# Optimization experiments

Measured on AMD Instinct MI355X. Metric: run time of the kernel, lower is better.

The kernel has to match this reference:

```python
import jax, jax.numpy as jnp
import numpy as np

N_HEAD = 16
EPS = 1e-5

def _layernorm(x, g, b):
    m = jnp.mean(x, axis=-1, keepdims=True)
    v = jnp.mean((x - m) ** 2, axis=-1, keepdims=True)
    return (x - m) * jax.lax.rsqrt(v + EPS) * g + b

def _gru_gate(h, X, w, u, bz):
    # w, u: [3, C, C] stacked (r, z, h) matrices; matches torch.tensordot(X, W, dims=1)
    r = jax.nn.sigmoid(X @ w[0] + h @ u[0])
    z = jax.nn.sigmoid(X @ w[1] + h @ u[1] - bz)
    h_next = jnp.tanh(X @ w[2] + (h * r) @ u[2])
    return (1.0 - z) * h + z * h_next

def setup_inputs() -> dict:
    key = jax.random.key(0)
    B, T, C = 4, 1024, 1024
    ks = jax.random.split(key, 32)
    s = 0.02
    inp = {
        'q': jax.random.normal(ks[0], (B, T, C), jnp.float32),
        'k': jax.random.normal(ks[1], (B, T, C), jnp.float32),
        'v': jax.random.normal(ks[2], (B, T, C), jnp.float32),
        'ln1_g': jnp.ones((C,), jnp.float32), 'ln1_b': jnp.zeros((C,), jnp.float32),
        'ln2_g': jnp.ones((C,), jnp.float32), 'ln2_b': jnp.zeros((C,), jnp.float32),
        'Wq': jax.random.normal(ks[3], (C, C), jnp.float32) * s, 'bq': jnp.zeros((C,), jnp.float32),
        'Wk': jax.random.normal(ks[4], (C, C), jnp.float32) * s, 'bk': jnp.zeros((C,), jnp.float32),
        'Wv': jax.random.normal(ks[5], (C, C), jnp.float32) * s, 'bv': jnp.zeros((C,), jnp.float32),
        'Wp': jax.random.normal(ks[6], (C, C), jnp.float32) * s, 'bp': jnp.zeros((C,), jnp.float32),
        'W1': jax.random.normal(ks[7], (C, 2 * C), jnp.float32) * s, 'b1': jnp.zeros((2 * C,), jnp.float32),
        'W2': jax.random.normal(ks[8], (2 * C, C), jnp.float32) * s, 'b2': jnp.zeros((C,), jnp.float32),
        'g1_w': jax.random.normal(ks[9], (3, C, C), jnp.float32) * s,
        'g1_u': jax.random.normal(ks[10], (3, C, C), jnp.float32) * s,
        'g1_bz': jnp.full((C,), 2.0, jnp.float32),  # init_gru_gate_bias
        'g2_w': jax.random.normal(ks[11], (3, C, C), jnp.float32) * s,
        'g2_u': jax.random.normal(ks[12], (3, C, C), jnp.float32) * s,
        'g2_bz': jnp.full((C,), 2.0, jnp.float32),
    }
    return inp

def reference(q, k, v, ln1_g, ln1_b, ln2_g, ln2_b, Wq, bq, Wk, bk, Wv, bv, Wp, bp,
              W1, b1, W2, b2, g1_w, g1_u, g1_bz, g2_w, g2_u, g2_bz):
    B, T, C = q.shape
    D = C // N_HEAD
    qn = _layernorm(q, ln1_g, ln1_b)
    kn = _layernorm(k, ln1_g, ln1_b)
    vn = _layernorm(v, ln1_g, ln1_b)
    qh = (qn @ Wq + bq).reshape(B, T, N_HEAD, D)
    kh = (kn @ Wk + bk).reshape(B, T, N_HEAD, D)
    vh = (vn @ Wv + bv).reshape(B, T, N_HEAD, D)
    att = jnp.einsum('bqhd,bkhd->bhqk', qh, kh) * (1.0 / np.sqrt(D))
    causal = jnp.tril(jnp.ones((T, T), bool))  # mask[-Tq:, :Tk]
    att_scores = jnp.where(causal, att, -jnp.inf)
    att_probs = jax.nn.softmax(att_scores, axis=-1)
    y = jnp.einsum('bhqk,bkhd->bqhd', att_probs, vh).reshape(B, T, C)
    att_out = y @ Wp + bp
    x = _gru_gate(q, att_out, g1_w, g1_u, g1_bz)
    h = _layernorm(x, ln2_g, ln2_b)
    mlp = jax.nn.gelu(h @ W1 + b1, approximate=False) @ W2 + b2
    x = _gru_gate(x, mlp, g2_w, g2_u, g2_bz)
    return (x, att_scores)
```

## Files before the change

### kernel.cpp

```cpp
#include <hip/hip_runtime.h>
#include <math.h>

#define TDIM 1024
#define CDIM 1024
#define NHEAD 16
#define HD 64
#define MROWS 4096

#define MASK_NEG -1.0e30f

typedef __attribute__((ext_vector_type(8))) __bf16 bf16x8;
typedef __attribute__((ext_vector_type(4))) float f32x4;

__device__ __forceinline__ float sigf(float x) { return 1.0f / (1.0f + expf(-x)); }
__device__ __forceinline__ float geluf(float x) { return x * 0.5f * (1.0f + erff(x * 0.7071067811865475f)); }
__device__ __forceinline__ float bf2f(unsigned short u) {
    union { unsigned u; float f; } x; x.u = ((unsigned)u) << 16; return x.f;
}
__device__ __forceinline__ unsigned short f2bf(float f) {
    union { float f; unsigned u; } x; x.f = f;
    unsigned r = x.u + 0x7FFFu + ((x.u >> 16) & 1u);
    return (unsigned short)(r >> 16);
}

__global__ __launch_bounds__(256) void wconv_t(const float* __restrict__ i0,
                                               const float* __restrict__ i1,
                                               const float* __restrict__ i2,
                                               const float* __restrict__ i3,
                                               int gper,
                                               unsigned short* __restrict__ out,
                                               int K, int N) {
    int z = blockIdx.z;
    int sel = z / gper, sub = z % gper;
    const float* ps = sel == 0 ? i0 : sel == 1 ? i1 : sel == 2 ? i2 : i3;
    const float* inb = ps + (size_t)sub * K * N;
    unsigned short* outb = out + (size_t)z * K * N;
    __shared__ float tile[32][33];
    int t = threadIdx.x;
    int r = t >> 3, c = (t & 7) * 4;
    int kb = blockIdx.y * 32, nb = blockIdx.x * 32;
    float4 vv = *(const float4*)(inb + (size_t)(kb + r) * N + nb + c);
    tile[r][c + 0] = vv.x; tile[r][c + 1] = vv.y; tile[r][c + 2] = vv.z; tile[r][c + 3] = vv.w;
    __syncthreads();
    ushort4 o;
    o.x = f2bf(tile[c + 0][r]); o.y = f2bf(tile[c + 1][r]);
    o.z = f2bf(tile[c + 2][r]); o.w = f2bf(tile[c + 3][r]);
    *(ushort4*)(outb + (size_t)(nb + r) * K + kb + c) = o;
}

__global__ __launch_bounds__(256) void f2bf_kernel(const float* __restrict__ in,
                                                   unsigned short* __restrict__ out) {
    size_t i = ((size_t)blockIdx.x * 256 + threadIdx.x) * 4;
    float4 v = *(const float4*)(in + i);
    ushort4 o; o.x = f2bf(v.x); o.y = f2bf(v.y); o.z = f2bf(v.z); o.w = f2bf(v.w);
    *(ushort4*)(out + i) = o;
}

__global__ __launch_bounds__(256) void ln3_kernel(const float* __restrict__ p0,
                                                  const float* __restrict__ p1,
                                                  const float* __restrict__ p2,
                                                  const float* __restrict__ g,
                                                  const float* __restrict__ b,
                                                  unsigned short* __restrict__ out) {
    int row = blockIdx.x, z = blockIdx.y;
    const float* xr = (z == 0 ? p0 : z == 1 ? p1 : p2) + (size_t)row * CDIM;
    int t = threadIdx.x;
    float4 v = *(const float4*)(xr + t * 4);
    __shared__ float red[256];
    red[t] = v.x + v.y + v.z + v.w;
    __syncthreads();
    for (int o = 128; o > 0; o >>= 1) { if (t < o) red[t] += red[t + o]; __syncthreads(); }
    float mean = red[0] * (1.0f / CDIM);
    __syncthreads();
    float dx = v.x - mean, dy = v.y - mean, dz = v.z - mean, dw = v.w - mean;
    red[t] = dx * dx + dy * dy + dz * dz + dw * dw;
    __syncthreads();
    for (int o = 128; o > 0; o >>= 1) { if (t < o) red[t] += red[t + o]; __syncthreads(); }
    float var = red[0] * (1.0f / CDIM);
    float inv = 1.0f / sqrtf(var + 1e-5f);
    float4 gv = *(const float4*)(g + t * 4);
    float4 bv = *(const float4*)(b + t * 4);
    ushort4 o4;
    o4.x = f2bf(dx * inv * gv.x + bv.x);
    o4.y = f2bf(dy * inv * gv.y + bv.y);
    o4.z = f2bf(dz * inv * gv.z + bv.z);
    o4.w = f2bf(dw * inv * gv.w + bv.w);
    *(ushort4*)(out + ((size_t)z * MROWS + row) * CDIM + t * 4) = o4;
}

template <int GELU>
__global__ __launch_bounds__(256) void mfma_gemm(const unsigned short* __restrict__ A0, size_t aStride,
                                                 const unsigned short* __restrict__ Bt0, size_t bStride,
                                                 const float* __restrict__ b0,
                                                 const float* __restrict__ b1,
                                                 const float* __restrict__ b2,
                                                 unsigned short* __restrict__ C0, size_t cStride,
                                                 int M, int N, int K, int outmode) {
    __shared__ unsigned short As[2][128 * 32];
    __shared__ unsigned short Bs[2][128 * 32];
    int z = blockIdx.z;
    const unsigned short* A = A0 + (size_t)z * aStride;
    const unsigned short* Bt = Bt0 + (size_t)z * bStride;
    unsigned short* C = C0 + (size_t)z * cStride;
    const float* bias = z == 0 ? b0 : z == 1 ? b1 : b2;
    int om = (outmode == 3) ? (z == 2 ? 2 : 1) : outmode;

    int t = threadIdx.x;
    int wave = t >> 6, lane = t & 63;
    int nwg = gridDim.x * gridDim.y;
    int hID = blockIdx.y * gridDim.x + blockIdx.x;
    int nl = (hID & 7) * (nwg >> 3) + (hID >> 3);
    int bx = nl % gridDim.x, by = nl / gridDim.x;
    int m0 = by * 128, n0 = bx * 128;
    int wx = wave & 1, wy = wave >> 1;
    int srow = lane >> 2;
    int scol = (lane & 3) * 8;
    int fr = lane & 15;
    int fq = (lane >> 4) * 8;

    f32x4 acc[4][4] = {};

#define STAGE_AB(buf, k0v)                                                                         \
    {                                                                                              \
        _Pragma("unroll")                                                                          \
        for (int i = 0; i < 2; i++) {                                                              \
            int rt = (wave * 2 + i) * 16 + srow;                                                   \
            __builtin_amdgcn_global_load_lds(                                                      \
                (const __attribute__((address_space(1))) void*)(A + (size_t)(m0 + rt) * K + (k0v) + scol), \
                (__attribute__((address_space(3))) void*)(As[buf] + rt * 32 + scol), 16, 0, 0);    \
            __builtin_amdgcn_global_load_lds(                                                      \
                (const __attribute__((address_space(1))) void*)(Bt + (size_t)(n0 + rt) * K + (k0v) + scol), \
                (__attribute__((address_space(3))) void*)(Bs[buf] + rt * 32 + scol), 16, 0, 0);    \
        }                                                                                          \
    }

    STAGE_AB(0, 0);
    int cur = 0;
    for (int k0 = 0; k0 < K; k0 += 32) {
        __syncthreads();
        if (k0 + 32 < K) STAGE_AB(cur ^ 1, k0 + 32);

        bf16x8 af[4], bfr[4];
#pragma unroll
        for (int mi = 0; mi < 4; mi++)
            af[mi] = *(const bf16x8*)(As[cur] + (wy * 64 + mi * 16 + fr) * 32 + fq);
#pragma unroll
        for (int ni = 0; ni < 4; ni++)
            bfr[ni] = *(const bf16x8*)(Bs[cur] + (wx * 64 + ni * 16 + fr) * 32 + fq);
#pragma unroll
        for (int mi = 0; mi < 4; mi++)
#pragma unroll
            for (int ni = 0; ni < 4; ni++)
                acc[mi][ni] = __builtin_amdgcn_mfma_f32_16x16x32_bf16(af[mi], bfr[ni], acc[mi][ni], 0, 0, 0);
        cur ^= 1;
    }
#undef STAGE_AB

    int col_l = lane & 15, quad = lane >> 4;
#pragma unroll
    for (int ni = 0; ni < 4; ni++) {
        int c = n0 + wx * 64 + ni * 16 + col_l;
        float bb = bias ? bias[c] : 0.0f;
#pragma unroll
        for (int mi = 0; mi < 4; mi++) {
#pragma unroll
            for (int r = 0; r < 4; r++) {
                int row = m0 + wy * 64 + mi * 16 + quad * 4 + r;
                float vv = acc[mi][ni][r] + bb;
                if (GELU) vv = geluf(vv);
                size_t idx;
                if (om == 1) {
                    int bI = row >> 10, tt2 = row & 1023, hh = c >> 6, d = c & 63;
                    idx = (((size_t)(bI * NHEAD + hh)) * TDIM + tt2) * HD + d;
                } else if (om == 2) {
                    int bI = row >> 10, tt2 = row & 1023, hh = c >> 6, d = c & 63;
                    idx = (((size_t)(bI * NHEAD + hh)) * HD + d) * TDIM + tt2;
                } else {
                    idx = (size_t)row * N + c;
                }
                C[idx] = f2bf(vv);
            }
        }
    }
}

__global__ __launch_bounds__(256, 4) void attn_fused(const unsigned short* __restrict__ Q,
                                                     const unsigned short* __restrict__ K,
                                                     const unsigned short* __restrict__ Vt,
                                                     float* __restrict__ S,
                                                     unsigned short* __restrict__ Y) {
    int hID = blockIdx.y * gridDim.x + blockIdx.x;
    int nlw = (hID & 7) * 128 + (hID >> 3);
    int qt = nlw & 15, bh = nlw >> 4;
    int q0 = qt * 64;
    int t = threadIdx.x, w = t >> 6, lane = t & 63;
    int l15 = lane & 15, quad = lane >> 4;
    int l7 = lane & 7, l3 = lane >> 3;

    __shared__ unsigned short Ks[2][4096];
    __shared__ unsigned short Vs[2][4096];
    __shared__ unsigned short PsU[4096];

    const unsigned short* Qb = Q + ((size_t)bh * TDIM + q0) * HD;
    const unsigned short* Kb0 = K + (size_t)bh * TDIM * HD;
    const unsigned short* Vtb = Vt + (size_t)bh * HD * TDIM;
    float* Sb = S + (size_t)bh * TDIM * TDIM;

    int dstoff = w * 512 + lane * 8;

    bf16x8 aq[2];
    {
        int qrow = w * 16 + l15;
#pragma unroll
        for (int kk = 0; kk < 2; kk++)
            aq[kk] = *(const bf16x8*)(Qb + (size_t)qrow * HD + kk * 32 + quad * 8);
    }

    float m_run[4], l_run[4];
    f32x4 yacc[4];
#pragma unroll
    for (int r = 0; r < 4; r++) { m_run[r] = MASK_NEG; l_run[r] = 0.f; }
#pragma unroll
    for (int nd = 0; nd < 4; nd++) yacc[nd] = (f32x4){0.f, 0.f, 0.f, 0.f};

    unsigned short* Psw = PsU + w * 1024;

#define STAGE_KV(buf, ktile)                                                                        \
    {                                                                                               \
        _Pragma("unroll")                                                                           \
        for (int it = 0; it < 2; it++) {                                                            \
            int row = it * 32 + w * 8 + l3;                                        \
            __builtin_amdgcn_global_load_lds(                                                       \
                (const __attribute__((address_space(1))) void*)(Kb0 + (size_t)((ktile) * 64 + row) * HD + ((l7 ^ l3) << 3)), \
                (__attribute__((address_space(3))) void*)(Ks[buf] + it * 2048 + dstoff), 16, 0, 0); \
            __builtin_amdgcn_global_load_lds(                                                       \
                (const __attribute__((address_space(1))) void*)(Vtb + (size_t)row * TDIM + (ktile) * 64 + ((l7 ^ l3) << 3)), \
                (__attribute__((address_space(3))) void*)(Vs[buf] + it * 2048 + dstoff), 16, 0, 0); \
        }                                                                                           \
    }

    STAGE_KV(0, 0);
    int cur = 0;

    for (int kt = 0; kt <= qt; kt++) {
        __syncthreads();
        if (kt < qt) STAGE_KV(cur ^ 1, kt + 1);

        f32x4 sA[4];
#pragma unroll
        for (int n = 0; n < 4; n++) sA[n] = (f32x4){0.f, 0.f, 0.f, 0.f};
        __builtin_amdgcn_s_setprio(1);
#pragma unroll
        for (int kk = 0; kk < 2; kk++) {
#pragma unroll
            for (int n = 0; n < 4; n++) {
                int krow = n * 16 + l15;
                bf16x8 bk = *(const bf16x8*)(Ks[cur] + krow * 64 + ((((kk * 64 + quad * 16)) ^ ((krow & 7) << 4)) >> 1));
                sA[n] = __builtin_amdgcn_mfma_f32_16x16x32_bf16(aq[kk], bk, sA[n], 0, 0, 0);
            }
        }
        __builtin_amdgcn_s_setprio(0);

        int kbase = kt * 64;
        bool diag = (kt == qt);
#pragma unroll
        for (int n = 0; n < 4; n++) {
            int kg = kbase + n * 16 + l15;
#pragma unroll
            for (int r = 0; r < 4; r++) {
                int qg = q0 + w * 16 + quad * 4 + r;
                float x = sA[n][r] * 0.125f;
                if (diag && kg > qg) x = MASK_NEG;
                sA[n][r] = x;
                Sb[(size_t)qg * TDIM + kg] = x;
            }
        }

#pragma unroll
        for (int r = 0; r < 4; r++) {
            float m = fmaxf(fmaxf(sA[0][r], sA[1][r]), fmaxf(sA[2][r], sA[3][r]));
            m = fmaxf(m, __shfl_xor(m, 1));
            m = fmaxf(m, __shfl_xor(m, 2));
            m = fmaxf(m, __shfl_xor(m, 4));
            m = fmaxf(m, __shfl_xor(m, 8));
            float mn = fmaxf(m_run[r], m);
            float sc = expf(m_run[r] - mn);
            m_run[r] = mn;
            float ls = 0.f;
#pragma unroll
            for (int n = 0; n < 4; n++) {
                float p = expf(sA[n][r] - mn);
                sA[n][r] = p;
                ls += p;
            }
            ls += __shfl_xor(ls, 1);
            ls += __shfl_xor(ls, 2);
            ls += __shfl_xor(ls, 4);
            ls += __shfl_xor(ls, 8);
            l_run[r] = l_run[r] * sc + ls;
#pragma unroll
            for (int nd = 0; nd < 4; nd++) yacc[nd][r] *= sc;
        }

#pragma unroll
        for (int n = 0; n < 4; n++) {
            int kk2 = n * 16 + l15;
#pragma unroll
            for (int r = 0; r < 4; r++) {
                int qq = quad * 4 + r;
                Psw[qq * 64 + (((kk2 * 2) ^ ((qq & 7) << 4)) >> 1)] = f2bf(sA[n][r]);
            }
        }

        __builtin_amdgcn_s_setprio(1);
#pragma unroll
        for (int kk = 0; kk < 2; kk++) {
            bf16x8 pa = *(const bf16x8*)(Psw + l15 * 64 + ((((kk * 64 + quad * 16)) ^ ((l15 & 7) << 4)) >> 1));
#pragma unroll
            for (int nd = 0; nd < 4; nd++) {
                int dr = nd * 16 + l15;
                bf16x8 bv = *(const bf16x8*)(Vs[cur] + dr * 64 + ((((kk * 64 + quad * 16)) ^ ((dr & 7) << 4)) >> 1));
                yacc[nd] = __builtin_amdgcn_mfma_f32_16x16x32_bf16(pa, bv, yacc[nd], 0, 0, 0);
            }
        }
        __builtin_amdgcn_s_setprio(0);
        cur ^= 1;
    }
#undef STAGE_KV

    int bI = bh >> 4, h = bh & 15;
#pragma unroll
    for (int r = 0; r < 4; r++) {
        float inv = 1.0f / l_run[r];
        int row = bI * TDIM + q0 + w * 16 + quad * 4 + r;
#pragma unroll
        for (int nd = 0; nd < 4; nd++)
            Y[(size_t)row * CDIM + h * HD + nd * 16 + l15] = f2bf(yacc[nd][r] * inv);
    }

    int kfill = (qt + 1) * 64;
    if (kfill < TDIM) {
        float4 m4 = make_float4(MASK_NEG, MASK_NEG, MASK_NEG, MASK_NEG);
        int rr = t >> 4, cc = (t & 15) * 4;
#pragma unroll
        for (int rp = 0; rp < 4; rp++) {
            float* Srow = Sb + (size_t)(q0 + rp * 16 + rr) * TDIM;
            for (int k4 = kfill + cc; k4 < TDIM; k4 += 64)
                *(float4*)(Srow + k4) = m4;
        }
    }
}

__global__ __launch_bounds__(256) void ew_r(const unsigned short* __restrict__ A, int ldA,
                                            const unsigned short* __restrict__ B, int ldB,
                                            const unsigned short* __restrict__ h,
                                            unsigned short* __restrict__ out) {
    int row = blockIdx.x, c = threadIdx.x * 4;
    ushort4 a = *(const ushort4*)(A + (size_t)row * ldA + c);
    ushort4 b = *(const ushort4*)(B + (size_t)row * ldB + c);
    size_t i = (size_t)row * CDIM + c;
    ushort4 hh = *(const ushort4*)(h + i);
    ushort4 o;
    o.x = f2bf(bf2f(hh.x) * sigf(bf2f(a.x) + bf2f(b.x)));
    o.y = f2bf(bf2f(hh.y) * sigf(bf2f(a.y) + bf2f(b.y)));
    o.z = f2bf(bf2f(hh.z) * sigf(bf2f(a.z) + bf2f(b.z)));
    o.w = f2bf(bf2f(hh.w) * sigf(bf2f(a.w) + bf2f(b.w)));
    *(ushort4*)(out + i) = o;
}

template <int F32OUT, int DOLN>
__global__ __launch_bounds__(256) void ew_final2(const unsigned short* __restrict__ A, int ldA,
                                                 const unsigned short* __restrict__ B, int ldB,
                                                 const unsigned short* __restrict__ B3v,
                                                 const unsigned short* __restrict__ h,
                                                 const float* __restrict__ bz,
                                                 void* __restrict__ out,
                                                 const float* __restrict__ lng,
                                                 const float* __restrict__ lnb,
                                                 unsigned short* __restrict__ lnout) {
    int row = blockIdx.x, t = threadIdx.x, c = t * 4;
    size_t ia = (size_t)row * ldA, ib = (size_t)row * ldB;
    size_t i = (size_t)row * CDIM + c;
    ushort4 a2 = *(const ushort4*)(A + ia + 1024 + c);
    ushort4 b2 = *(const ushort4*)(B + ib + 1024 + c);
    ushort4 a3 = *(const ushort4*)(A + ia + 2048 + c);
    ushort4 b3 = *(const ushort4*)(B3v + i);
    ushort4 hh = *(const ushort4*)(h + i);
    float4 bzv = *(const float4*)(bz + c);
    float zz, o0, o1, o2, o3;
    zz = sigf(bf2f(a2.x) + bf2f(b2.x) - bzv.x); o0 = (1.f - zz) * bf2f(hh.x) + zz * tanhf(bf2f(a3.x) + bf2f(b3.x));
    zz = sigf(bf2f(a2.y) + bf2f(b2.y) - bzv.y); o1 = (1.f - zz) * bf2f(hh.y) + zz * tanhf(bf2f(a3.y) + bf2f(b3.y));
    zz = sigf(bf2f(a2.z) + bf2f(b2.z) - bzv.z); o2 = (1.f - zz) * bf2f(hh.z) + zz * tanhf(bf2f(a3.z) + bf2f(b3.z));
    zz = sigf(bf2f(a2.w) + bf2f(b2.w) - bzv.w); o3 = (1.f - zz) * bf2f(hh.w) + zz * tanhf(bf2f(a3.w) + bf2f(b3.w));
    if (F32OUT) {
        *(float4*)((float*)out + i) = make_float4(o0, o1, o2, o3);
    } else {
        ushort4 o; o.x = f2bf(o0); o.y = f2bf(o1); o.z = f2bf(o2); o.w = f2bf(o3);
        *(ushort4*)((unsigned short*)out + i) = o;
    }
    if (DOLN) {
        __shared__ float red[256];
        red[t] = o0 + o1 + o2 + o3;
        __syncthreads();
        for (int o = 128; o > 0; o >>= 1) { if (t < o) red[t] += red[t + o]; __syncthreads(); }
        float mean = red[0] * (1.0f / CDIM);
        __syncthreads();
        float dx = o0 - mean, dy = o1 - mean, dz = o2 - mean, dw = o3 - mean;
        red[t] = dx * dx + dy * dy + dz * dz + dw * dw;
        __syncthreads();
        for (int o = 128; o > 0; o >>= 1) { if (t < o) red[t] += red[t + o]; __syncthreads(); }
        float var = red[0] * (1.0f / CDIM);
        float inv = 1.0f / sqrtf(var + 1e-5f);
        float4 gv = *(const float4*)(lng + c);
        float4 bv = *(const float4*)(lnb + c);
        ushort4 o4;
        o4.x = f2bf(dx * inv * gv.x + bv.x);
        o4.y = f2bf(dy * inv * gv.y + bv.y);
        o4.z = f2bf(dz * inv * gv.z + bv.z);
        o4.w = f2bf(dw * inv * gv.w + bv.w);
        *(ushort4*)(lnout + i) = o4;
    }
}

extern "C" void kernel_launch(void* const* d_in, const int* in_sizes, int n_in,
                              void* d_out, int out_size, void* d_ws, size_t ws_size,
                              hipStream_t stream) {
    const float* q    = (const float*)d_in[0];
    const float* k    = (const float*)d_in[1];
    const float* v    = (const float*)d_in[2];
    const float* ln1g = (const float*)d_in[3];
    const float* ln1b = (const float*)d_in[4];
    const float* ln2g = (const float*)d_in[5];
    const float* ln2b = (const float*)d_in[6];
    const float* Wq   = (const float*)d_in[7];
    const float* bq   = (const float*)d_in[8];
    const float* Wk   = (const float*)d_in[9];
    const float* bk   = (const float*)d_in[10];
    const float* Wv   = (const float*)d_in[11];
    const float* bv   = (const float*)d_in[12];
    const float* Wp   = (const float*)d_in[13];
    const float* bp   = (const float*)d_in[14];
    const float* W1   = (const float*)d_in[15];
    const float* b1   = (const float*)d_in[16];
    const float* W2   = (const float*)d_in[17];
    const float* b2   = (const float*)d_in[18];
    const float* g1w  = (const float*)d_in[19];
    const float* g1u  = (const float*)d_in[20];
    const float* g1bz = (const float*)d_in[21];
    const float* g2w  = (const float*)d_in[22];
    const float* g2u  = (const float*)d_in[23];
    const float* g2bz = (const float*)d_in[24];

    float* out_x = (float*)d_out;
    float* out_s = out_x + (size_t)MROWS * CDIM;

    unsigned short* w = (unsigned short*)d_ws;
    const size_t MM = (size_t)CDIM * CDIM;
    unsigned short* wWq  = w;
    unsigned short* wWp  = w + 3 * MM;
    unsigned short* wW1  = w + 4 * MM;
    unsigned short* wW2  = w + 6 * MM;
    unsigned short* wg1w = w + 8 * MM;
    unsigned short* wg1u = w + 11 * MM;
    unsigned short* wg2w = w + 14 * MM;
    unsigned short* wg2u = w + 17 * MM;
    unsigned short* act = w + 20 * MM;
    const size_t SLOT = (size_t)MROWS * CDIM;
    unsigned short* s0 = act + 0 * SLOT;
    unsigned short* s1 = act + 1 * SLOT;
    unsigned short* s2 = act + 2 * SLOT;
    unsigned short* s3 = act + 3 * SLOT;
    unsigned short* s4 = act + 4 * SLOT;
    unsigned short* s5 = act + 5 * SLOT;
    unsigned short* s6 = act + 6 * SLOT;
    unsigned short* s7 = act + 7 * SLOT;
    unsigned short* s8 = act + 8 * SLOT;
    (void)s4;

    dim3 blk(256);
    dim3 g_gemm(8, 32, 1);
    dim3 g_gemm3(8, 32, 3);
    dim3 g_gemm_w1(16, 32, 1);
    dim3 g_gemm_g(24, 32, 1);
    dim3 g_attn(16, 64);
    dim3 g_ew(MROWS);

    wconv_t<<<dim3(32, 32, 4), blk, 0, stream>>>(Wq, Wk, Wv, Wp, 1, wWq, 1024, 1024);
    wconv_t<<<dim3(32, 32, 12), blk, 0, stream>>>(g1w, g1u, g2w, g2u, 3, wg1w, 1024, 1024);
    wconv_t<<<dim3(64, 32, 1), blk, 0, stream>>>(W1, W1, W1, W1, 1, wW1, 1024, 2048);
    wconv_t<<<dim3(32, 64, 1), blk, 0, stream>>>(W2, W2, W2, W2, 1, wW2, 2048, 1024);
    f2bf_kernel<<<g_ew, blk, 0, stream>>>(q, s6);

    ln3_kernel<<<dim3(MROWS, 3), blk, 0, stream>>>(q, k, v, ln1g, ln1b, s0);
    mfma_gemm<0><<<g_gemm3, blk, 0, stream>>>(s0, SLOT, wWq, MM, bq, bk, bv, s3, SLOT,
                                              MROWS, CDIM, CDIM, 3);

    attn_fused<<<g_attn, blk, 0, stream>>>(s3, s4, s5, out_s, s0);

    mfma_gemm<0><<<g_gemm, blk, 0, stream>>>(s0, 0, wWp, 0, bp, bp, bp, s1, 0,
                                             MROWS, CDIM, CDIM, 0);

    mfma_gemm<0><<<g_gemm_g, blk, 0, stream>>>(s1, 0, wg1w, 0, nullptr, nullptr, nullptr,
                                               s2, 0, MROWS, 3 * CDIM, CDIM, 0);
    mfma_gemm<0><<<g_gemm_w1, blk, 0, stream>>>(s6, 0, wg1u, 0, nullptr, nullptr, nullptr,
                                                s0, 0, MROWS, 2 * CDIM, CDIM, 0);
    ew_r<<<g_ew, blk, 0, stream>>>(s2, 3 * CDIM, s0, 2 * CDIM, s6, s5);
    mfma_gemm<0><<<g_gemm, blk, 0, stream>>>(s5, 0, wg1u + 2 * MM, 0, nullptr, nullptr, nullptr,
                                             s7, 0, MROWS, CDIM, CDIM, 0);
    ew_final2<0, 1><<<g_ew, blk, 0, stream>>>(s2, 3 * CDIM, s0, 2 * CDIM, s7, s6, g1bz,
                                              s5, ln2g, ln2b, s8);

    mfma_gemm<1><<<g_gemm_w1, blk, 0, stream>>>(s8, 0, wW1, 0, b1, b1, b1, s0, 0,
                                                MROWS, 2 * CDIM, CDIM, 0);
    mfma_gemm<0><<<g_gemm, blk, 0, stream>>>(s0, 0, wW2, 0, b2, b2, b2, s6, 0,
                                             MROWS, CDIM, 2 * CDIM, 0);

    mfma_gemm<0><<<g_gemm_g, blk, 0, stream>>>(s6, 0, wg2w, 0, nullptr, nullptr, nullptr,
                                               s0, 0, MROWS, 3 * CDIM, CDIM, 0);
    mfma_gemm<0><<<g_gemm_w1, blk, 0, stream>>>(s5, 0, wg2u, 0, nullptr, nullptr, nullptr,
                                                s3, 0, MROWS, 2 * CDIM, CDIM, 0);
    ew_r<<<g_ew, blk, 0, stream>>>(s0, 3 * CDIM, s3, 2 * CDIM, s5, s7);
    mfma_gemm<0><<<g_gemm, blk, 0, stream>>>(s7, 0, wg2u + 2 * MM, 0, nullptr, nullptr, nullptr,
                                             s8, 0, MROWS, CDIM, CDIM, 0);
    ew_final2<1, 0><<<g_ew, blk, 0, stream>>>(s0, 3 * CDIM, s3, 2 * CDIM, s8, s5, g2bz,
                                              out_x, nullptr, nullptr, nullptr);
}
```

Baseline: 909.8 us.

## Batch independent GEMMs via per-z descriptor kernel and fuse q bf16 conversion into LN

Replaces the templated GEMM with a descriptor-driven kernel in which each grid z-slice has its own A, B, bias, output, stride, layout mode and GELU flag. Independent GEMMs are merged into single launches: the QKV projections together with the h@U_r/U_z products of gate 1, and the W1 MLP GEMM together with the gate-2 h@U_r/U_z products. The q-to-bf16 conversion is folded into the layernorm kernel, and the buffers are reassigned so the gate products are written to separate contiguous slots. The aim is fewer launches and larger grids that fill the GPU better, at the cost of runtime branching on GELU and layout mode in the GEMM epilogue.

Result: no change. 909.5 us (-0.0%).

```diff
diff --git a/kernel.cpp b/kernel.cpp
--- a/kernel.cpp
+++ b/kernel.cpp
@@ -48,24 +48,21 @@
     *(ushort4*)(outb + (size_t)(nb + r) * K + kb + c) = o;
 }
 
-__global__ __launch_bounds__(256) void f2bf_kernel(const float* __restrict__ in,
-                                                   unsigned short* __restrict__ out) {
-    size_t i = ((size_t)blockIdx.x * 256 + threadIdx.x) * 4;
-    float4 v = *(const float4*)(in + i);
-    ushort4 o; o.x = f2bf(v.x); o.y = f2bf(v.y); o.z = f2bf(v.z); o.w = f2bf(v.w);
-    *(ushort4*)(out + i) = o;
-}
-
 __global__ __launch_bounds__(256) void ln3_kernel(const float* __restrict__ p0,
                                                   const float* __restrict__ p1,
                                                   const float* __restrict__ p2,
                                                   const float* __restrict__ g,
                                                   const float* __restrict__ b,
-                                                  unsigned short* __restrict__ out) {
+                                                  unsigned short* __restrict__ out,
+                                                  unsigned short* __restrict__ qb) {
     int row = blockIdx.x, z = blockIdx.y;
     const float* xr = (z == 0 ? p0 : z == 1 ? p1 : p2) + (size_t)row * CDIM;
     int t = threadIdx.x;
     float4 v = *(const float4*)(xr + t * 4);
+    if (z == 0) {
+        ushort4 o; o.x = f2bf(v.x); o.y = f2bf(v.y); o.z = f2bf(v.z); o.w = f2bf(v.w);
+        *(ushort4*)(qb + (size_t)row * CDIM + t * 4) = o;
+    }
     __shared__ float red[256];
     red[t] = v.x + v.y + v.z + v.w;
     __syncthreads();
@@ -88,22 +85,31 @@
     *(ushort4*)(out + ((size_t)z * MROWS + row) * CDIM + t * 4) = o4;
 }
 
-template <int GELU>
-__global__ __launch_bounds__(256) void mfma_gemm(const unsigned short* __restrict__ A0, size_t aStride,
-                                                 const unsigned short* __restrict__ Bt0, size_t bStride,
-                                                 const float* __restrict__ b0,
-                                                 const float* __restrict__ b1,
-                                                 const float* __restrict__ b2,
-                                                 unsigned short* __restrict__ C0, size_t cStride,
-                                                 int M, int N, int K, int outmode) {
+struct GemmZ {
+    const unsigned short* A;
+    const unsigned short* Bt;
+    const float* bias;
+    unsigned short* C;
+    int ldC;
+    int om;
+    int gelu;
+    int pad;
+};
+struct GemmDesc { GemmZ z0, z1, z2, z3, z4; };
+
+__global__ __launch_bounds__(256) void mfma_gemmz(GemmDesc d, int M, int N, int K) {
     __shared__ unsigned short As[2][128 * 32];
     __shared__ unsigned short Bs[2][128 * 32];
-    int z = blockIdx.z;
-    const unsigned short* A = A0 + (size_t)z * aStride;
-    const unsigned short* Bt = Bt0 + (size_t)z * bStride;
-    unsigned short* C = C0 + (size_t)z * cStride;
-    const float* bias = z == 0 ? b0 : z == 1 ? b1 : b2;
-    int om = (outmode == 3) ? (z == 2 ? 2 : 1) : outmode;
+    GemmZ zz;
+    switch (blockIdx.z) {
+        case 0: zz = d.z0; break;
+        case 1: zz = d.z1; break;
+        case 2: zz = d.z2; break;
+        case 3: zz = d.z3; break;
+        default: zz = d.z4; break;
+    }
+    const unsigned short* A = zz.A;
+    const unsigned short* Bt = zz.Bt;
 
     int t = threadIdx.x;
     int wave = t >> 6, lane = t & 63;
@@ -160,25 +166,25 @@
 #pragma unroll
     for (int ni = 0; ni < 4; ni++) {
         int c = n0 + wx * 64 + ni * 16 + col_l;
-        float bb = bias ? bias[c] : 0.0f;
+        float bb = zz.bias ? zz.bias[c] : 0.0f;
 #pragma unroll
         for (int mi = 0; mi < 4; mi++) {
 #pragma unroll
             for (int r = 0; r < 4; r++) {
                 int row = m0 + wy * 64 + mi * 16 + quad * 4 + r;
                 float vv = acc[mi][ni][r] + bb;
-                if (GELU) vv = geluf(vv);
+                if (zz.gelu) vv = geluf(vv);
                 size_t idx;
-                if (om == 1) {
-                    int bI = row >> 10, tt2 = row & 1023, hh = c >> 6, d = c & 63;
-                    idx = (((size_t)(bI * NHEAD + hh)) * TDIM + tt2) * HD + d;
-                } else if (om == 2) {
-                    int bI = row >> 10, tt2 = row & 1023, hh = c >> 6, d = c & 63;
-                    idx = (((size_t)(bI * NHEAD + hh)) * HD + d) * TDIM + tt2;
+                if (zz.om == 1) {
+                    int bI = row >> 10, tt2 = row & 1023, hh = c >> 6, dd = c & 63;
+                    idx = (((size_t)(bI * NHEAD + hh)) * TDIM + tt2) * HD + dd;
+                } else if (zz.om == 2) {
+                    int bI = row >> 10, tt2 = row & 1023, hh = c >> 6, dd = c & 63;
+                    idx = (((size_t)(bI * NHEAD + hh)) * HD + dd) * TDIM + tt2;
                 } else {
-                    idx = (size_t)row * N + c;
+                    idx = (size_t)row * zz.ldC + c;
                 }
-                C[idx] = f2bf(vv);
+                zz.C[idx] = f2bf(vv);
             }
         }
     }
@@ -351,14 +357,14 @@
     }
 }
 
-__global__ __launch_bounds__(256) void ew_r(const unsigned short* __restrict__ A, int ldA,
-                                            const unsigned short* __restrict__ B, int ldB,
+__global__ __launch_bounds__(256) void ew_r(const unsigned short* __restrict__ A1, int ldA,
+                                            const unsigned short* __restrict__ B1,
                                             const unsigned short* __restrict__ h,
                                             unsigned short* __restrict__ out) {
     int row = blockIdx.x, c = threadIdx.x * 4;
-    ushort4 a = *(const ushort4*)(A + (size_t)row * ldA + c);
-    ushort4 b = *(const ushort4*)(B + (size_t)row * ldB + c);
+    ushort4 a = *(const ushort4*)(A1 + (size_t)row * ldA + c);
     size_t i = (size_t)row * CDIM + c;
+    ushort4 b = *(const ushort4*)(B1 + i);
     ushort4 hh = *(const ushort4*)(h + i);
     ushort4 o;
     o.x = f2bf(bf2f(hh.x) * sigf(bf2f(a.x) + bf2f(b.x)));
@@ -370,7 +376,7 @@
 
 template <int F32OUT, int DOLN>
 __global__ __launch_bounds__(256) void ew_final2(const unsigned short* __restrict__ A, int ldA,
-                                                 const unsigned short* __restrict__ B, int ldB,
+                                                 const unsigned short* __restrict__ B2p,
                                                  const unsigned short* __restrict__ B3v,
                                                  const unsigned short* __restrict__ h,
                                                  const float* __restrict__ bz,
@@ -379,10 +385,10 @@
                                                  const float* __restrict__ lnb,
                                                  unsigned short* __restrict__ lnout) {
     int row = blockIdx.x, t = threadIdx.x, c = t * 4;
-    size_t ia = (size_t)row * ldA, ib = (size_t)row * ldB;
+    size_t ia = (size_t)row * ldA;
     size_t i = (size_t)row * CDIM + c;
     ushort4 a2 = *(const ushort4*)(A + ia + 1024 + c);
-    ushort4 b2 = *(const ushort4*)(B + ib + 1024 + c);
+    ushort4 b2 = *(const ushort4*)(B2p + i);
     ushort4 a3 = *(const ushort4*)(A + ia + 2048 + c);
     ushort4 b3 = *(const ushort4*)(B3v + i);
     ushort4 hh = *(const ushort4*)(h + i);
@@ -457,6 +463,8 @@
     unsigned short* w = (unsigned short*)d_ws;
     const size_t MM = (size_t)CDIM * CDIM;
     unsigned short* wWq  = w;
+    unsigned short* wWk  = w + 1 * MM;
+    unsigned short* wWv  = w + 2 * MM;
     unsigned short* wWp  = w + 3 * MM;
     unsigned short* wW1  = w + 4 * MM;
     unsigned short* wW2  = w + 6 * MM;
@@ -475,53 +483,94 @@
     unsigned short* s6 = act + 6 * SLOT;
     unsigned short* s7 = act + 7 * SLOT;
     unsigned short* s8 = act + 8 * SLOT;
-    (void)s4;
+    (void)s4; (void)wWk; (void)wWv;
 
     dim3 blk(256);
-    dim3 g_gemm(8, 32, 1);
-    dim3 g_gemm3(8, 32, 3);
-    dim3 g_gemm_w1(16, 32, 1);
-    dim3 g_gemm_g(24, 32, 1);
     dim3 g_attn(16, 64);
     dim3 g_ew(MROWS);
+
+    auto mkz = [](const unsigned short* A, const unsigned short* Bt, const float* bias,
+                  unsigned short* C, int ldC, int om, int gelu) {
+        GemmZ z; z.A = A; z.Bt = Bt; z.bias = bias; z.C = C; z.ldC = ldC; z.om = om;
+        z.gelu = gelu; z.pad = 0; return z;
+    };
 
     wconv_t<<<dim3(32, 32, 4), blk, 0, stream>>>(Wq, Wk, Wv, Wp, 1, wWq, 1024, 1024);
     wconv_t<<<dim3(32, 32, 12), blk, 0, stream>>>(g1w, g1u, g2w, g2u, 3, wg1w, 1024, 1024);
     wconv_t<<<dim3(64, 32, 1), blk, 0, stream>>>(W1, W1, W1, W1, 1, wW1, 1024, 2048);
     wconv_t<<<dim3(32, 64, 1), blk, 0, stream>>>(W2, W2, W2, W2, 1, wW2, 2048, 1024);
-    f2bf_kernel<<<g_ew, blk, 0, stream>>>(q, s6);
-
-    ln3_kernel<<<dim3(MROWS, 3), blk, 0, stream>>>(q, k, v, ln1g, ln1b, s0);
-    mfma_gemm<0><<<g_gemm3, blk, 0, stream>>>(s0, SLOT, wWq, MM, bq, bk, bv, s3, SLOT,
-                                              MROWS, CDIM, CDIM, 3);
+
+    ln3_kernel<<<dim3(MROWS, 3), blk, 0, stream>>>(q, k, v, ln1g, ln1b, s0, s6);
+
+    {
+        GemmDesc dd = { mkz(s0, wWq, bq, s3, 0, 1, 0),
+                        mkz(s1, wWq + 1 * MM, bk, s4, 0, 1, 0),
+                        mkz(s2, wWq + 2 * MM, bv, s5, 0, 2, 0),
+                        mkz(s6, wg1u + 0 * MM, nullptr, s7, CDIM, 0, 0),
+                        mkz(s6, wg1u + 1 * MM, nullptr, s8, CDIM, 0, 0) };
+        mfma_gemmz<<<dim3(8, 32, 5), blk, 0, stream>>>(dd, MROWS, CDIM, CDIM);
+    }
 
     attn_fused<<<g_attn, blk, 0, stream>>>(s3, s4, s5, out_s, s0);
 
-    mfma_gemm<0><<<g_gemm, blk, 0, stream>>>(s0, 0, wWp, 0, bp, bp, bp, s1, 0,
-                                             MROWS, CDIM, CDIM, 0);
-
-    mfma_gemm<0><<<g_gemm_g, blk, 0, stream>>>(s1, 0, wg1w, 0, nullptr, nullptr, nullptr,
-                                               s2, 0, MROWS, 3 * CDIM, CDIM, 0);
-    mfma_gemm<0><<<g_gemm_w1, blk, 0, stream>>>(s6, 0, wg1u, 0, nullptr, nullptr, nullptr,
-                                                s0, 0, MROWS, 2 * CDIM, CDIM, 0);
-    ew_r<<<g_ew, blk, 0, stream>>>(s2, 3 * CDIM, s0, 2 * CDIM, s6, s5);
-    mfma_gemm<0><<<g_gemm, blk, 0, stream>>>(s5, 0, wg1u + 2 * MM, 0, nullptr, nullptr, nullptr,
-                                             s7, 0, MROWS, CDIM, CDIM, 0);
-    ew_final2<0, 1><<<g_ew, blk, 0, stream>>>(s2, 3 * CDIM, s0, 2 * CDIM, s7, s6, g1bz,
-                                              s5, ln2g, ln2b, s8);
-
-    mfma_gemm<1><<<g_gemm_w1, blk, 0, stream>>>(s8, 0, wW1, 0, b1, b1, b1, s0, 0,
-                                                MROWS, 2 * CDIM, CDIM, 0);
-    mfma_gemm<0><<<g_gemm, blk, 0, stream>>>(s0, 0, wW2, 0, b2, b2, b2, s6, 0,
-                                             MROWS, CDIM, 2 * CDIM, 0);
-
-    mfma_gemm<0><<<g_gemm_g, blk, 0, stream>>>(s6, 0, wg2w, 0, nullptr, nullptr, nullptr,
-                                               s0, 0, MROWS, 3 * CDIM, CDIM, 0);
-    mfma_gemm<0><<<g_gemm_w1, blk, 0, stream>>>(s5, 0, wg2u, 0, nullptr, nullptr, nullptr,
-                                                s3, 0, MROWS, 2 * CDIM, CDIM, 0);
-    ew_r<<<g_ew, blk, 0, stream>>>(s0, 3 * CDIM, s3, 2 * CDIM, s5, s7);
-    mfma_gemm<0><<<g_gemm, blk, 0, stream>>>(s7, 0, wg2u + 2 * MM, 0, nullptr, nullptr, nullptr,
-                                             s8, 0, MROWS, CDIM, CDIM, 0);
-    ew_final2<1, 0><<<g_ew, blk, 0, stream>>>(s0, 3 * CDIM, s3, 2 * CDIM, s8, s5, g2bz,
+    {
+        GemmDesc dd = { mkz(s0, wWp, bp, s1, CDIM, 0, 0),
+                        mkz(s0, wWp, bp, s1, CDIM, 0, 0), mkz(s0, wWp, bp, s1, CDIM, 0, 0),
+                        mkz(s0, wWp, bp, s1, CDIM, 0, 0), mkz(s0, wWp, bp, s1, CDIM, 0, 0) };
+        mfma_gemmz<<<dim3(8, 32, 1), blk, 0, stream>>>(dd, MROWS, CDIM, CDIM);
+    }
+
+    {
+        GemmDesc dd = { mkz(s1, wg1w + 0 * MM, nullptr, s2, 3 * CDIM, 0, 0),
+                        mkz(s1, wg1w + 1 * MM, nullptr, s2 + CDIM, 3 * CDIM, 0, 0),
+                        mkz(s1, wg1w + 2 * MM, nullptr, s2 + 2 * CDIM, 3 * CDIM, 0, 0),
+                        mkz(s1, wg1w, nullptr, s2, 3 * CDIM, 0, 0),
+                        mkz(s1, wg1w, nullptr, s2, 3 * CDIM, 0, 0) };
+        mfma_gemmz<<<dim3(8, 32, 3), blk, 0, stream>>>(dd, MROWS, CDIM, CDIM);
+    }
+    ew_r<<<g_ew, blk, 0, stream>>>(s2, 3 * CDIM, s7, s6, s5);
+    {
+        GemmDesc dd = { mkz(s5, wg1u + 2 * MM, nullptr, s0, CDIM, 0, 0),
+                        mkz(s5, wg1u + 2 * MM, nullptr, s0, CDIM, 0, 0),
+                        mkz(s5, wg1u + 2 * MM, nullptr, s0, CDIM, 0, 0),
+                        mkz(s5, wg1u + 2 * MM, nullptr, s0, CDIM, 0, 0),
+                        mkz(s5, wg1u + 2 * MM, nullptr, s0, CDIM, 0, 0) };
+        mfma_gemmz<<<dim3(8, 32, 1), blk, 0, stream>>>(dd, MROWS, CDIM, CDIM);
+    }
+    ew_final2<0, 1><<<g_ew, blk, 0, stream>>>(s2, 3 * CDIM, s8, s0, s6, g1bz,
+                                              s1, ln2g, ln2b, s5);
+
+    {
+        GemmDesc dd = { mkz(s5, wW1, b1, s3, 2 * CDIM, 0, 1),
+                        mkz(s5, wW1 + MM, b1 + 1024, s3 + CDIM, 2 * CDIM, 0, 1),
+                        mkz(s1, wg2u + 0 * MM, nullptr, s6, CDIM, 0, 0),
+                        mkz(s1, wg2u + 1 * MM, nullptr, s7, CDIM, 0, 0),
+                        mkz(s5, wW1, b1, s3, 2 * CDIM, 0, 1) };
+        mfma_gemmz<<<dim3(8, 32, 4), blk, 0, stream>>>(dd, MROWS, CDIM, CDIM);
+    }
+    {
+        GemmDesc dd = { mkz(s3, wW2, b2, s0, CDIM, 0, 0),
+                        mkz(s3, wW2, b2, s0, CDIM, 0, 0), mkz(s3, wW2, b2, s0, CDIM, 0, 0),
+                        mkz(s3, wW2, b2, s0, CDIM, 0, 0), mkz(s3, wW2, b2, s0, CDIM, 0, 0) };
+        mfma_gemmz<<<dim3(8, 32, 1), blk, 0, stream>>>(dd, MROWS, CDIM, 2 * CDIM);
+    }
+    {
+        GemmDesc dd = { mkz(s0, wg2w + 0 * MM, nullptr, s2, 3 * CDIM, 0, 0),
+                        mkz(s0, wg2w + 1 * MM, nullptr, s2 + CDIM, 3 * CDIM, 0, 0),
+                        mkz(s0, wg2w + 2 * MM, nullptr, s2 + 2 * CDIM, 3 * CDIM, 0, 0),
+                        mkz(s0, wg2w, nullptr, s2, 3 * CDIM, 0, 0),
+                        mkz(s0, wg2w, nullptr, s2, 3 * CDIM, 0, 0) };
+        mfma_gemmz<<<dim3(8, 32, 3), blk, 0, stream>>>(dd, MROWS, CDIM, CDIM);
+    }
+    ew_r<<<g_ew, blk, 0, stream>>>(s2, 3 * CDIM, s6, s1, s5);
+    {
+        GemmDesc dd = { mkz(s5, wg2u + 2 * MM, nullptr, s8, CDIM, 0, 0),
+                        mkz(s5, wg2u + 2 * MM, nullptr, s8, CDIM, 0, 0),
+                        mkz(s5, wg2u + 2 * MM, nullptr, s8, CDIM, 0, 0),
+                        mkz(s5, wg2u + 2 * MM, nullptr, s8, CDIM, 0, 0),
+                        mkz(s5, wg2u + 2 * MM, nullptr, s8, CDIM, 0, 0) };
+        mfma_gemmz<<<dim3(8, 32, 1), blk, 0, stream>>>(dd, MROWS, CDIM, CDIM);
+    }
+    ew_final2<1, 0><<<g_ew, blk, 0, stream>>>(s2, 3 * CDIM, s7, s8, s1, g2bz,
                                               out_x, nullptr, nullptr, nullptr);
 }
```
